# Kernel optimization log

Hardware: AMD Instinct MI355X
Metric: run time of the kernel (lower is better)

Reference implementation:

```python
import jax, jax.numpy as jnp
import numpy as np

K, S, PAD = 3, 2, 1
C, HID = 16, 128
H, W = 256, 256
EPS = 1e-6


def _unfold(xp, k, s):
    # xp: (B, C, Hp, Wp) -> (B, C*k*k, L), torch.nn.Unfold ordering (c major, then kh, kw)
    B, Cc, Hp, Wp = xp.shape
    Ho = (Hp - k) // s + 1
    Wo = (Wp - k) // s + 1
    cols = jnp.stack(
        [xp[:, :, i:i + (Ho - 1) * s + 1:s, j:j + (Wo - 1) * s + 1:s]
         for i in range(k) for j in range(k)], axis=2)  # (B, C, k*k, Ho, Wo)
    return cols.reshape(B, Cc * k * k, Ho * Wo), Ho, Wo


def _fold(patches, Hp, Wp, Ho, Wo, k, s):
    # patches: (B, C*k*k, L) -> scatter-add into (B, C, Hp, Wp)
    B = patches.shape[0]
    p = patches.reshape(B, -1, k, k, Ho, Wo)
    out = jnp.zeros((B, p.shape[1], Hp, Wp), dtype=patches.dtype)
    for i in range(k):
        for j in range(k):
            out = out.at[:, :, i:i + (Ho - 1) * s + 1:s, j:j + (Wo - 1) * s + 1:s].add(p[:, :, i, j])
    return out


def setup_inputs() -> dict:
    key = jax.random.key(0)
    ks = jax.random.split(key, 7)
    P = C * K * K  # 144
    x = jax.random.normal(ks[0], (32, C, H, W), dtype=jnp.float32)
    W1 = jax.random.normal(ks[1], (P, HID), dtype=jnp.float32) * (1.0 / np.sqrt(P))
    b1 = jax.random.normal(ks[2], (HID,), dtype=jnp.float32) * 0.01
    W2 = jax.random.normal(ks[3], (HID, P), dtype=jnp.float32) * (1.0 / np.sqrt(HID))
    b2 = jax.random.normal(ks[4], (P,), dtype=jnp.float32) * 0.01
    Wc = jax.random.normal(ks[5], (C, C), dtype=jnp.float32) * (1.0 / np.sqrt(C))
    bc = jax.random.normal(ks[6], (C,), dtype=jnp.float32) * 0.01
    return {"x": x, "W1": W1, "b1": b1, "W2": W2, "b2": b2, "Wc": Wc, "bc": bc}


def reference(x, W1, b1, W2, b2, Wc, bc):
    Hp, Wp = H + 2 * PAD, W + 2 * PAD
    xp = jnp.pad(x, ((0, 0), (0, 0), (PAD, PAD), (PAD, PAD)), mode='reflect')
    patches, Ho, Wo = _unfold(xp, K, S)          # (B, P, L)
    t = patches.transpose(0, 2, 1)               # (B, L, P)
    hcat = jax.nn.relu(t @ W1 + b1)              # (B, L, HID)
    out_p = (hcat @ W2 + b2).transpose(0, 2, 1)  # (B, P, L)
    folded = _fold(out_p, Hp, Wp, Ho, Wo, K, S)
    counts = _fold(jnp.ones_like(out_p), Hp, Wp, Ho, Wo, K, S)
    normalized = folded / (counts + EPS)
    logits = jnp.einsum('oc,bchw->bohw', Wc, normalized) + bc[None, :, None, None]
    attn = jax.nn.softmax(logits, axis=1)        # Softmax2d = softmax over channels
    modulated = normalized * attn
    return modulated[:, :, PAD:PAD + H, PAD:PAD + W]
```

## Files before the change

kernel.cpp:

```cpp
#include <hip/hip_runtime.h>
#include <math.h>

#define CC   16
#define HH   256
#define WW   256
#define HIDN 128
#define PDIM 144
#define K1PAD 160
#define PITCH_H 136

typedef _Float16 half8 __attribute__((ext_vector_type(8)));
typedef float   f32x4 __attribute__((ext_vector_type(4)));

#define MFMA16(a, b, c) __builtin_amdgcn_mfma_f32_16x16x32_f16((a), (b), (c), 0, 0, 0)

#define O_BYTES   ((size_t)524288 * 144 * 2)
#define W1T_OFF   O_BYTES
#define W1T_BYTES ((size_t)128 * K1PAD * 2)
#define W2T_OFF   (W1T_OFF + W1T_BYTES)
#define W2T_BYTES ((size_t)144 * 128 * 2)
#define WS_NEEDED (W2T_OFF + W2T_BYTES)

__device__ __forceinline__ void load_lds16(const float* g, float* l)
{
#if __has_builtin(__builtin_amdgcn_global_load_lds)
    __builtin_amdgcn_global_load_lds(
        (const __attribute__((address_space(1))) unsigned int*)g,
        (__attribute__((address_space(3))) unsigned int*)l, 16, 0, 0);
#else
    *(float4*)l = *(const float4*)g;
#endif
}

__global__ __launch_bounds__(256) void prep_kernel(
    const float* __restrict__ W1, const float* __restrict__ W2,
    _Float16* __restrict__ W1T, _Float16* __restrict__ W2T)
{
    const int idx = blockIdx.x * 256 + threadIdx.x;
    if (idx < 128 * K1PAD) {
        const int n = idx / K1PAD;
        const int k = idx - n * K1PAD;
        const int tap = k >> 4;
        const int c   = k & 15;
        W1T[idx] = (tap < 9) ? (_Float16)W1[(c * 9 + tap) * HIDN + n] : (_Float16)0.f;
    }
    if (idx < 144 * 128) {
        const int nn = idx >> 7;
        const int k  = idx & 127;
        const int tap = nn >> 4;
        const int c   = nn & 15;
        W2T[nn * 128 + k] = (_Float16)W2[k * PDIM + (c * 9 + tap)];
    }
}

__global__ __launch_bounds__(256) void mlp_kernel(
    const float* __restrict__ x,
    const _Float16* __restrict__ W1T, const float* __restrict__ b1,
    const _Float16* __restrict__ W2T, const float* __restrict__ b2,
    _Float16* __restrict__ og)
{
    __shared__ __align__(16) char smem[73728];
    _Float16* xT    = (_Float16*)smem;
    float*    xrowF = (float*)(smem + 24576);
    _Float16* hT    = (_Float16*)(smem + 24576);

    const int tid   = threadIdx.x;
    const int a     = blockIdx.x & 127;
    const int batch = blockIdx.x >> 7;
    const float* xb = x + (size_t)batch * CC * HH * WW;

    #pragma unroll
    for (int it = 0; it < 12; ++it) {
        const int idx = tid + it * 256;
        const int i   = idx >> 10;
        const int c   = (idx >> 6) & 15;
        const int q   = idx & 63;
        int ym = 2 * a + i - 1;
        if (ym < 0) ym = 1;
        load_lds16(xb + ((c * HH + ym) * WW + 4 * q), xrowF + idx * 4);
    }
    __syncthreads();

    #pragma unroll
    for (int k = 0; k < 3; ++k) {
        const int u  = tid + k * 256;
        const int i  = u >> 8;
        const int xm = u & 255;
        const float* rbase = xrowF + i * 4096 + xm;
        half8 lo, hi;
        #pragma unroll
        for (int c = 0; c < 8; ++c) lo[c] = (_Float16)rbase[c * 256];
        #pragma unroll
        for (int c = 0; c < 8; ++c) hi[c] = (_Float16)rbase[(c + 8) * 256];
        int s = u << 4;
        s ^= (s & 64) >> 3;
        *(half8*)(xT + s)       = lo;
        *(half8*)(xT + (s ^ 8)) = hi;
    }
    __syncthreads();

    const int wid  = tid >> 6;
    const int lane = tid & 63;
    const int l15  = lane & 15;
    const int quad = lane >> 4;
    const int qh   = quad >> 1;
    const int c0   = (quad & 1) * 8;

    {
        half8 bfr0[5], bfr1[5];
        float bias0, bias1;
        {
            const int nt0 = 2 * wid, nt1 = 2 * wid + 1;
            const _Float16* w0 = W1T + (nt0 * 16 + l15) * K1PAD + quad * 8;
            const _Float16* w1 = W1T + (nt1 * 16 + l15) * K1PAD + quad * 8;
            #pragma unroll
            for (int ks = 0; ks < 5; ++ks) {
                bfr0[ks] = *(const half8*)(w0 + ks * 32);
                bfr1[ks] = *(const half8*)(w1 + ks * 32);
            }
            bias0 = b1[nt0 * 16 + l15];
            bias1 = b1[nt1 * 16 + l15];
        }
        int koffU[5], koffF[5];
        #pragma unroll
        for (int ks = 0; ks < 5; ++ks) {
            int tap = 2 * ks + qh;
            if (tap > 8) tap = 8;
            const int i   = (tap * 11) >> 5;
            const int j   = tap - 3 * i;
            const int xmU = 2 * l15 + j - 1;
            const int xmF = (xmU < 0) ? 1 : xmU;
            koffU[ks] = (i << 12) + (xmU << 4) + c0;
            koffF[ks] = (i << 12) + (xmF << 4) + c0;
        }

        #define G1_STEP(MT, KO)                                                   \
        {                                                                         \
            f32x4 acc0 = {0.f, 0.f, 0.f, 0.f};                                    \
            f32x4 acc1 = {0.f, 0.f, 0.f, 0.f};                                    \
            _Pragma("unroll")                                                     \
            for (int ks = 0; ks < 5; ++ks) {                                      \
                int ix = KO[ks] + ((MT) << 9);                                    \
                ix ^= (ix & 64) >> 3;                                             \
                const half8 af = *(const half8*)(xT + ix);                        \
                acc0 = MFMA16(af, bfr0[ks], acc0);                                \
                acc1 = MFMA16(af, bfr1[ks], acc1);                                \
            }                                                                     \
            _Pragma("unroll")                                                     \
            for (int r = 0; r < 4; ++r) {                                         \
                const int row = (MT) * 16 + quad * 4 + r;                         \
                float h0 = acc0[r] + bias0;                                       \
                float h1 = acc1[r] + bias1;                                       \
                hT[row * PITCH_H + (2 * wid) * 16 + l15]     = (_Float16)(h0 > 0.f ? h0 : 0.f); \
                hT[row * PITCH_H + (2 * wid + 1) * 16 + l15] = (_Float16)(h1 > 0.f ? h1 : 0.f); \
            }                                                                     \
        }

        G1_STEP(0, koffF)
        for (int mt = 1; mt < 8; ++mt) G1_STEP(mt, koffU)
        #undef G1_STEP
    }
    __syncthreads();

    const size_t abase = ((size_t)batch * 128 + a) * 9;
    for (int nt = wid; nt < 9; nt += 4) {
        half8 bfr2[4];
        const _Float16* w2row = W2T + (nt * 16 + l15) * 128 + quad * 8;
        #pragma unroll
        for (int ks = 0; ks < 4; ++ks)
            bfr2[ks] = *(const half8*)(w2row + ks * 32);
        const float bias2 = b2[l15 * 9 + nt];
        _Float16* ogn = og + (abase + nt) * 2048;
        for (int mt = 0; mt < 8; ++mt) {
            f32x4 acc = {0.f, 0.f, 0.f, 0.f};
            const _Float16* arow = hT + (mt * 16 + l15) * PITCH_H + quad * 8;
            #pragma unroll
            for (int ks = 0; ks < 4; ++ks)
                acc = MFMA16(*(const half8*)(arow + ks * 32), bfr2[ks], acc);
            #pragma unroll
            for (int r = 0; r < 4; ++r) {
                const int b = mt * 16 + quad * 4 + r;
                ogn[b * 16 + l15] = (_Float16)(acc[r] + bias2);
            }
        }
    }
}

__global__ __launch_bounds__(256) void gather_kernel(
    const _Float16* __restrict__ og, const float* __restrict__ Wc,
    const float* __restrict__ bc, float* __restrict__ out)
{
    __shared__ float sWc[256];
    __shared__ float sbc[16];
    const int tid = threadIdx.x;
    sWc[tid] = Wc[tid];
    if (tid < 16) sbc[tid] = bc[tid];
    __syncthreads();

    const int x     = tid;
    const int y     = blockIdx.x & 255;
    const int batch = blockIdx.x >> 8;

    int alist[2], ilist[2], na = 0;
    if ((y + 1) & 1) { alist[0] = y >> 1; ilist[0] = 1; na = 1; }
    else {
        if (y < 255) { alist[na] = (y + 1) >> 1; ilist[na] = 0; ++na; }
        alist[na] = (y - 1) >> 1; ilist[na] = 2; ++na;
    }
    int blist[2], jlist[2], nb = 0;
    if ((x + 1) & 1) { blist[0] = x >> 1; jlist[0] = 1; nb = 1; }
    else {
        if (x < 255) { blist[nb] = (x + 1) >> 1; jlist[nb] = 0; ++nb; }
        blist[nb] = (x - 1) >> 1; jlist[nb] = 2; ++nb;
    }

    float nrm[CC];
    #pragma unroll
    for (int c = 0; c < CC; ++c) nrm[c] = 0.f;

    const size_t pb = (size_t)batch * 128;
    for (int u = 0; u < 2; ++u) {
        if (u >= na) break;
        for (int v = 0; v < 2; ++v) {
            if (v >= nb) break;
            const int tap = ilist[u] * 3 + jlist[v];
            const _Float16* orow =
                og + (((pb + alist[u]) * 9 + tap) * 128 + blist[v]) * 16;
            const half8 o0 = *(const half8*)(orow);
            const half8 o1 = *(const half8*)(orow + 8);
            #pragma unroll
            for (int e = 0; e < 8; ++e) { nrm[e] += (float)o0[e]; nrm[8 + e] += (float)o1[e]; }
        }
    }
    const float inv = 1.f / ((float)(na * nb) + 1e-6f);
    #pragma unroll
    for (int c = 0; c < CC; ++c) nrm[c] *= inv;

    float lg[CC];
    #pragma unroll
    for (int o = 0; o < CC; ++o) {
        float s = sbc[o];
        #pragma unroll
        for (int c = 0; c < CC; ++c) s = fmaf(sWc[o * CC + c], nrm[c], s);
        lg[o] = s;
    }
    float mx = lg[0];
    #pragma unroll
    for (int o = 1; o < CC; ++o) mx = fmaxf(mx, lg[o]);
    float se = 0.f;
    #pragma unroll
    for (int o = 0; o < CC; ++o) { lg[o] = expf(lg[o] - mx); se += lg[o]; }
    const float isum = 1.f / se;

    const size_t obase = ((size_t)batch * CC) * (HH * WW) + (size_t)y * WW + x;
    #pragma unroll
    for (int c = 0; c < CC; ++c)
        out[obase + (size_t)c * (HH * WW)] = nrm[c] * lg[c] * isum;
}

#define HT_PITCH 68
__global__ __launch_bounds__(256) void mlp_fold_kernel_fb(
    const float* __restrict__ x,  const float* __restrict__ W1,
    const float* __restrict__ b1, const float* __restrict__ W2,
    const float* __restrict__ b2, float* __restrict__ folded)
{
    __shared__ __align__(16) float pT[PDIM * 64];
    __shared__ __align__(16) float hT[HIDN * HT_PITCH];
    const int tid = threadIdx.x;
    const int tile = blockIdx.x & 255;
    const int b = blockIdx.x >> 8;
    const int tile_base = tile * 64;
    const float* xb = x + (size_t)b * CC * HH * WW;
    for (int idx = tid; idx < PDIM * 64; idx += 256) {
        const int p = idx >> 6, lo = idx & 63;
        const int c = p / 9, rem = p - c * 9, i = rem / 3, j = rem - i * 3;
        const int l = tile_base + lo, a = l >> 7, bb = l & 127;
        int ym = 2 * a + i - 1, xm = 2 * bb + j - 1;
        if (ym < 0) ym = 1;
        if (xm < 0) xm = 1;
        pT[p * 64 + lo] = xb[(c * HH + ym) * WW + xm];
    }
    __syncthreads();
    {
        const int cg = tid & 31, rg = tid >> 5, rbase = rg * 8;
        float acc[8][4];
        #pragma unroll
        for (int m = 0; m < 8; ++m)
            #pragma unroll
            for (int jj = 0; jj < 4; ++jj) acc[m][jj] = 0.f;
        for (int k = 0; k < PDIM; ++k) {
            const float4 w = *reinterpret_cast<const float4*>(W1 + k * HIDN + cg * 4);
            const float4 pa = *reinterpret_cast<const float4*>(pT + k * 64 + rbase);
            const float4 pb2 = *reinterpret_cast<const float4*>(pT + k * 64 + rbase + 4);
            const float pv[8] = {pa.x, pa.y, pa.z, pa.w, pb2.x, pb2.y, pb2.z, pb2.w};
            const float wv[4] = {w.x, w.y, w.z, w.w};
            #pragma unroll
            for (int m = 0; m < 8; ++m)
                #pragma unroll
                for (int jj = 0; jj < 4; ++jj) acc[m][jj] = fmaf(pv[m], wv[jj], acc[m][jj]);
        }
        #pragma unroll
        for (int jj = 0; jj < 4; ++jj) {
            const int jcol = cg * 4 + jj;
            const float bj = b1[jcol];
            #pragma unroll
            for (int m = 0; m < 8; ++m) {
                const float hval = acc[m][jj] + bj;
                hT[jcol * HT_PITCH + rbase + m] = hval > 0.f ? hval : 0.f;
            }
        }
    }
    __syncthreads();
    {
        const int cg2 = tid & 15, rg2 = tid >> 4, rb2 = rg2 * 4;
        float acc2[4][9];
        #pragma unroll
        for (int m = 0; m < 4; ++m)
            #pragma unroll
            for (int jj = 0; jj < 9; ++jj) acc2[m][jj] = 0.f;
        const float* w2base = W2 + cg2 * 9;
        for (int h = 0; h < HIDN; ++h) {
            const float4 hv4 = *reinterpret_cast<const float4*>(hT + h * HT_PITCH + rb2);
            const float hv[4] = {hv4.x, hv4.y, hv4.z, hv4.w};
            float wv[9];
            #pragma unroll
            for (int jj = 0; jj < 9; ++jj) wv[jj] = w2base[h * PDIM + jj];
            #pragma unroll
            for (int m = 0; m < 4; ++m)
                #pragma unroll
                for (int jj = 0; jj < 9; ++jj) acc2[m][jj] = fmaf(hv[m], wv[jj], acc2[m][jj]);
        }
        float bv[9];
        #pragma unroll
        for (int jj = 0; jj < 9; ++jj) bv[jj] = b2[cg2 * 9 + jj];
        float* fb = folded + ((size_t)b * CC + cg2) * (HH * WW);
        #pragma unroll
        for (int m = 0; m < 4; ++m) {
            const int l = tile_base + rb2 + m, a = l >> 7, bb = l & 127;
            #pragma unroll
            for (int jj = 0; jj < 9; ++jj) {
                const int i = jj / 3, j2 = jj - i * 3;
                const int ypad = 2 * a + i, xpad = 2 * bb + j2;
                if (ypad >= 1 && xpad >= 1)
                    atomicAdd(fb + (ypad - 1) * WW + (xpad - 1), acc2[m][jj] + bv[jj]);
            }
        }
    }
}

__global__ __launch_bounds__(256) void norm_softmax_kernel_fb(
    float* __restrict__ out, const float* __restrict__ Wc, const float* __restrict__ bc)
{
    const int xo = threadIdx.x, yo = blockIdx.x & 255, b = blockIdx.x >> 8;
    const int yp = yo + 1, xp = xo + 1;
    const float cy = ((yp & 1) || yp == 256) ? 1.f : 2.f;
    const float cx = ((xp & 1) || xp == 256) ? 1.f : 2.f;
    const float inv = 1.f / (cy * cx + 1e-6f);
    const size_t base = ((size_t)b * CC) * (HH * WW) + (size_t)yo * WW + xo;
    float nrm[CC];
    #pragma unroll
    for (int c = 0; c < CC; ++c) nrm[c] = out[base + (size_t)c * (HH * WW)] * inv;
    float logits[CC];
    #pragma unroll
    for (int o = 0; o < CC; ++o) {
        float s = bc[o];
        #pragma unroll
        for (int c = 0; c < CC; ++c) s = fmaf(Wc[o * CC + c], nrm[c], s);
        logits[o] = s;
    }
    float mx = logits[0];
    #pragma unroll
    for (int o = 1; o < CC; ++o) mx = fmaxf(mx, logits[o]);
    float se = 0.f;
    #pragma unroll
    for (int o = 0; o < CC; ++o) { logits[o] = expf(logits[o] - mx); se += logits[o]; }
    const float isum = 1.f / se;
    #pragma unroll
    for (int c = 0; c < CC; ++c)
        out[base + (size_t)c * (HH * WW)] = nrm[c] * logits[c] * isum;
}

extern "C" void kernel_launch(void* const* d_in, const int* in_sizes, int n_in,
                              void* d_out, int out_size, void* d_ws, size_t ws_size,
                              hipStream_t stream)
{
    const float* x  = (const float*)d_in[0];
    const float* W1 = (const float*)d_in[1];
    const float* b1 = (const float*)d_in[2];
    const float* W2 = (const float*)d_in[3];
    const float* b2 = (const float*)d_in[4];
    const float* Wc = (const float*)d_in[5];
    const float* bc = (const float*)d_in[6];
    float* out = (float*)d_out;

    if (ws_size >= WS_NEEDED) {
        _Float16* og  = (_Float16*)d_ws;
        _Float16* W1T = (_Float16*)((char*)d_ws + W1T_OFF);
        _Float16* W2T = (_Float16*)((char*)d_ws + W2T_OFF);

        prep_kernel<<<dim3(80), dim3(256), 0, stream>>>(W1, W2, W1T, W2T);
        mlp_kernel<<<dim3(32 * 128), dim3(256), 0, stream>>>(x, W1T, b1, W2T, b2, og);
        gather_kernel<<<dim3(32 * 256), dim3(256), 0, stream>>>(og, Wc, bc, out);
    } else {
        hipMemsetAsync(d_out, 0, (size_t)out_size * sizeof(float), stream);
        mlp_fold_kernel_fb<<<dim3(32 * 256), dim3(256), 0, stream>>>(x, W1, b1, W2, b2, out);
        norm_softmax_kernel_fb<<<dim3(32 * 256), dim3(256), 0, stream>>>(out, Wc, bc);
    }
}
```

Before: 330.8 us.

## Double MLP block size to 512 threads and stage gather patch rows in LDS

```diff
diff --git a/kernel.cpp b/kernel.cpp
--- a/kernel.cpp
+++ b/kernel.cpp
@@ -8,6 +8,7 @@
 #define PDIM 144
 #define K1PAD 160
 #define PITCH_H 136
+#define PP 2056
 
 typedef _Float16 half8 __attribute__((ext_vector_type(8)));
 typedef float   f32x4 __attribute__((ext_vector_type(4)));
@@ -32,6 +33,17 @@
 #endif
 }
 
+__device__ __forceinline__ void load_lds16h(const _Float16* g, _Float16* l)
+{
+#if __has_builtin(__builtin_amdgcn_global_load_lds)
+    __builtin_amdgcn_global_load_lds(
+        (const __attribute__((address_space(1))) unsigned int*)g,
+        (__attribute__((address_space(3))) unsigned int*)l, 16, 0, 0);
+#else
+    *(float4*)(void*)l = *(const float4*)(const void*)g;
+#endif
+}
+
 __global__ __launch_bounds__(256) void prep_kernel(
     const float* __restrict__ W1, const float* __restrict__ W2,
     _Float16* __restrict__ W1T, _Float16* __restrict__ W2T)
@@ -53,7 +65,7 @@
     }
 }
 
-__global__ __launch_bounds__(256) void mlp_kernel(
+__global__ __launch_bounds__(512) void mlp_kernel(
     const float* __restrict__ x,
     const _Float16* __restrict__ W1T, const float* __restrict__ b1,
     const _Float16* __restrict__ W2T, const float* __restrict__ b2,
@@ -70,8 +82,8 @@
     const float* xb = x + (size_t)batch * CC * HH * WW;
 
     #pragma unroll
-    for (int it = 0; it < 12; ++it) {
-        const int idx = tid + it * 256;
+    for (int it = 0; it < 6; ++it) {
+        const int idx = tid + it * 512;
         const int i   = idx >> 10;
         const int c   = (idx >> 6) & 15;
         const int q   = idx & 63;
@@ -82,20 +94,22 @@
     __syncthreads();
 
     #pragma unroll
-    for (int k = 0; k < 3; ++k) {
-        const int u  = tid + k * 256;
-        const int i  = u >> 8;
-        const int xm = u & 255;
-        const float* rbase = xrowF + i * 4096 + xm;
-        half8 lo, hi;
-        #pragma unroll
-        for (int c = 0; c < 8; ++c) lo[c] = (_Float16)rbase[c * 256];
-        #pragma unroll
-        for (int c = 0; c < 8; ++c) hi[c] = (_Float16)rbase[(c + 8) * 256];
-        int s = u << 4;
-        s ^= (s & 64) >> 3;
-        *(half8*)(xT + s)       = lo;
-        *(half8*)(xT + (s ^ 8)) = hi;
+    for (int k = 0; k < 2; ++k) {
+        const int u = tid + k * 512;
+        if (u < 768) {
+            const int i  = u >> 8;
+            const int xm = u & 255;
+            const float* rbase = xrowF + i * 4096 + xm;
+            half8 lo, hi;
+            #pragma unroll
+            for (int c = 0; c < 8; ++c) lo[c] = (_Float16)rbase[c * 256];
+            #pragma unroll
+            for (int c = 0; c < 8; ++c) hi[c] = (_Float16)rbase[(c + 8) * 256];
+            int s = u << 4;
+            s ^= (s & 0x1C0) >> 3;
+            *(half8*)(xT + s)       = lo;
+            *(half8*)(xT + (s ^ 8)) = hi;
+        }
     }
     __syncthreads();
 
@@ -105,12 +119,14 @@
     const int quad = lane >> 4;
     const int qh   = quad >> 1;
     const int c0   = (quad & 1) * 8;
+    const int wm   = wid >> 2;
+    const int wn   = wid & 3;
 
     {
         half8 bfr0[5], bfr1[5];
         float bias0, bias1;
         {
-            const int nt0 = 2 * wid, nt1 = 2 * wid + 1;
+            const int nt0 = 2 * wn, nt1 = 2 * wn + 1;
             const _Float16* w0 = W1T + (nt0 * 16 + l15) * K1PAD + quad * 8;
             const _Float16* w1 = W1T + (nt1 * 16 + l15) * K1PAD + quad * 8;
             #pragma unroll
@@ -141,7 +157,7 @@
             _Pragma("unroll")                                                     \
             for (int ks = 0; ks < 5; ++ks) {                                      \
                 int ix = KO[ks] + ((MT) << 9);                                    \
-                ix ^= (ix & 64) >> 3;                                             \
+                ix ^= (ix & 0x1C0) >> 3;                                          \
                 const half8 af = *(const half8*)(xT + ix);                        \
                 acc0 = MFMA16(af, bfr0[ks], acc0);                                \
                 acc1 = MFMA16(af, bfr1[ks], acc1);                                \
@@ -151,36 +167,75 @@
                 const int row = (MT) * 16 + quad * 4 + r;                         \
                 float h0 = acc0[r] + bias0;                                       \
                 float h1 = acc1[r] + bias1;                                       \
-                hT[row * PITCH_H + (2 * wid) * 16 + l15]     = (_Float16)(h0 > 0.f ? h0 : 0.f); \
-                hT[row * PITCH_H + (2 * wid + 1) * 16 + l15] = (_Float16)(h1 > 0.f ? h1 : 0.f); \
+                hT[row * PITCH_H + (2 * wn) * 16 + l15]     = (_Float16)(h0 > 0.f ? h0 : 0.f); \
+                hT[row * PITCH_H + (2 * wn + 1) * 16 + l15] = (_Float16)(h1 > 0.f ? h1 : 0.f); \
             }                                                                     \
         }
 
-        G1_STEP(0, koffF)
-        for (int mt = 1; mt < 8; ++mt) G1_STEP(mt, koffU)
+        if (wm == 0) {
+            G1_STEP(0, koffF)
+            #pragma unroll
+            for (int mt = 1; mt < 4; ++mt) G1_STEP(mt, koffU)
+        } else {
+            #pragma unroll
+            for (int mt = 4; mt < 8; ++mt) G1_STEP(mt, koffU)
+        }
         #undef G1_STEP
     }
     __syncthreads();
 
     const size_t abase = ((size_t)batch * 128 + a) * 9;
-    for (int nt = wid; nt < 9; nt += 4) {
-        half8 bfr2[4];
-        const _Float16* w2row = W2T + (nt * 16 + l15) * 128 + quad * 8;
-        #pragma unroll
-        for (int ks = 0; ks < 4; ++ks)
-            bfr2[ks] = *(const half8*)(w2row + ks * 32);
-        const float bias2 = b2[l15 * 9 + nt];
-        _Float16* ogn = og + (abase + nt) * 2048;
-        for (int mt = 0; mt < 8; ++mt) {
+    {
+        half8 bfr2[2][4];
+        float bias2[2];
+        #pragma unroll
+        for (int n = 0; n < 2; ++n) {
+            const int nt = 2 * wn + n;
+            const _Float16* w2row = W2T + (nt * 16 + l15) * 128 + quad * 8;
+            #pragma unroll
+            for (int ks = 0; ks < 4; ++ks)
+                bfr2[n][ks] = *(const half8*)(w2row + ks * 32);
+            bias2[n] = b2[l15 * 9 + nt];
+        }
+        _Float16* ognA = og + (abase + 2 * wn) * 2048;
+        _Float16* ognB = og + (abase + 2 * wn + 1) * 2048;
+        #pragma unroll
+        for (int m = 0; m < 4; ++m) {
+            const int mt = wm * 4 + m;
+            f32x4 acc0 = {0.f, 0.f, 0.f, 0.f};
+            f32x4 acc1 = {0.f, 0.f, 0.f, 0.f};
+            const _Float16* arow = hT + (mt * 16 + l15) * PITCH_H + quad * 8;
+            #pragma unroll
+            for (int ks = 0; ks < 4; ++ks) {
+                const half8 af = *(const half8*)(arow + ks * 32);
+                acc0 = MFMA16(af, bfr2[0][ks], acc0);
+                acc1 = MFMA16(af, bfr2[1][ks], acc1);
+            }
+            #pragma unroll
+            for (int r = 0; r < 4; ++r) {
+                const int b = mt * 16 + quad * 4 + r;
+                ognA[b * 16 + l15] = (_Float16)(acc0[r] + bias2[0]);
+                ognB[b * 16 + l15] = (_Float16)(acc1[r] + bias2[1]);
+            }
+        }
+        {
+            half8 bfr8[4];
+            const _Float16* w2row = W2T + (8 * 16 + l15) * 128 + quad * 8;
+            #pragma unroll
+            for (int ks = 0; ks < 4; ++ks)
+                bfr8[ks] = *(const half8*)(w2row + ks * 32);
+            const float bias8 = b2[l15 * 9 + 8];
+            _Float16* ogn = og + (abase + 8) * 2048;
+            const int mt = wid;
             f32x4 acc = {0.f, 0.f, 0.f, 0.f};
             const _Float16* arow = hT + (mt * 16 + l15) * PITCH_H + quad * 8;
             #pragma unroll
             for (int ks = 0; ks < 4; ++ks)
-                acc = MFMA16(*(const half8*)(arow + ks * 32), bfr2[ks], acc);
+                acc = MFMA16(*(const half8*)(arow + ks * 32), bfr8[ks], acc);
             #pragma unroll
             for (int r = 0; r < 4; ++r) {
                 const int b = mt * 16 + quad * 4 + r;
-                ogn[b * 16 + l15] = (_Float16)(acc[r] + bias2);
+                ogn[b * 16 + l15] = (_Float16)(acc[r] + bias8);
             }
         }
     }
@@ -190,16 +245,16 @@
     const _Float16* __restrict__ og, const float* __restrict__ Wc,
     const float* __restrict__ bc, float* __restrict__ out)
 {
+    __shared__ __align__(16) _Float16 sPl[6 * PP];
     __shared__ float sWc[256];
     __shared__ float sbc[16];
-    const int tid = threadIdx.x;
+
+    const int tid   = threadIdx.x;
+    const int y     = blockIdx.x & 255;
+    const int batch = blockIdx.x >> 8;
+
     sWc[tid] = Wc[tid];
     if (tid < 16) sbc[tid] = bc[tid];
-    __syncthreads();
-
-    const int x     = tid;
-    const int y     = blockIdx.x & 255;
-    const int batch = blockIdx.x >> 8;
 
     int alist[2], ilist[2], na = 0;
     if ((y + 1) & 1) { alist[0] = y >> 1; ilist[0] = 1; na = 1; }
@@ -207,6 +262,18 @@
         if (y < 255) { alist[na] = (y + 1) >> 1; ilist[na] = 0; ++na; }
         alist[na] = (y - 1) >> 1; ilist[na] = 2; ++na;
     }
+
+    const size_t pb = (size_t)batch * 128;
+    for (int p = 0; p < na * 3; ++p) {
+        const int u   = (p >= 3) ? 1 : 0;
+        const int j   = p - 3 * u;
+        const int tap = ilist[u] * 3 + j;
+        const _Float16* src = og + ((pb + alist[u]) * 9 + tap) * 2048 + tid * 8;
+        load_lds16h(src, sPl + p * PP + tid * 8);
+    }
+    __syncthreads();
+
+    const int x = tid;
     int blist[2], jlist[2], nb = 0;
     if ((x + 1) & 1) { blist[0] = x >> 1; jlist[0] = 1; nb = 1; }
     else {
@@ -218,14 +285,11 @@
     #pragma unroll
     for (int c = 0; c < CC; ++c) nrm[c] = 0.f;
 
-    const size_t pb = (size_t)batch * 128;
     for (int u = 0; u < 2; ++u) {
         if (u >= na) break;
         for (int v = 0; v < 2; ++v) {
             if (v >= nb) break;
-            const int tap = ilist[u] * 3 + jlist[v];
-            const _Float16* orow =
-                og + (((pb + alist[u]) * 9 + tap) * 128 + blist[v]) * 16;
+            const _Float16* orow = sPl + (u * 3 + jlist[v]) * PP + blist[v] * 16;
             const half8 o0 = *(const half8*)(orow);
             const half8 o1 = *(const half8*)(orow + 8);
             #pragma unroll
@@ -399,7 +463,7 @@
         _Float16* W2T = (_Float16*)((char*)d_ws + W2T_OFF);
 
         prep_kernel<<<dim3(80), dim3(256), 0, stream>>>(W1, W2, W1T, W2T);
-        mlp_kernel<<<dim3(32 * 128), dim3(256), 0, stream>>>(x, W1T, b1, W2T, b2, og);
+        mlp_kernel<<<dim3(32 * 128), dim3(512), 0, stream>>>(x, W1T, b1, W2T, b2, og);
         gather_kernel<<<dim3(32 * 256), dim3(256), 0, stream>>>(og, Wc, bc, out);
     } else {
         hipMemsetAsync(d_out, 0, (size_t)out_size * sizeof(float), stream);
```

Result: slower. 349.5 us (+5.7%).
